# Performance work log

Hardware: AMD Instinct MI355X
Metric: run time of the kernel (lower is better)

Reference implementation:

```python
import jax, jax.numpy as jnp
import numpy as np
import math

B, N, R = 1024, 50, 1000
N_POIS = 50000
D = 128
K_T = 64
K_D = 64
T_MAX = 10080.0
D_MAX = 200.0
EARTH_RADIUS_KM = 6371.0
DEG2RAD = math.pi / 180.0


def _interp_scalar(table, x):
    # Linear interpolation into 1-D table [K]; x are bin positions in [0, K-1].
    K = table.shape[0]
    x = jnp.clip(x, 0.0, K - 1 - 1e-06)
    k = jnp.floor(x).astype(jnp.int32)
    frac = x - k.astype(x.dtype)
    return (1.0 - frac) * table[k] + frac * table[jnp.minimum(k + 1, K - 1)]


def _haversine_km(lat1, lon1, lat2, lon2):
    dlat = (lat2 - lat1) * DEG2RAD
    dlon = (lon2 - lon1) * DEG2RAD
    a = jnp.sin(dlat / 2) ** 2 + jnp.cos(lat1 * DEG2RAD) * jnp.cos(lat2 * DEG2RAD) * jnp.sin(dlon / 2) ** 2
    a = jnp.clip(a, 0.0, 1.0)
    return EARTH_RADIUS_KM * 2.0 * jnp.arcsin(jnp.sqrt(a))


def setup_inputs() -> dict:
    key = jax.random.key(0)
    ks = jax.random.split(key, 16)
    poi_idx = jax.random.randint(ks[0], (B, N), 0, N_POIS)
    hour_of_week = jax.random.randint(ks[1], (B, N), 0, 169)
    lat = jax.random.uniform(ks[2], (B, N), jnp.float32)  # ~1 degree spread => up to ~150 km pairwise
    lon = jax.random.uniform(ks[3], (B, N), jnp.float32)
    t_min = jax.random.uniform(ks[4], (B, N), jnp.float32) * T_MAX
    region_centroids = jax.random.uniform(ks[5], (R, 2), jnp.float32)
    poi_emb = 0.02 * jax.random.normal(ks[6], (N_POIS + 1, D), jnp.float32)
    poi_emb = poi_emb.at[N_POIS].set(0.0)  # padding row
    time_emb = 0.02 * jax.random.normal(ks[7], (169, D), jnp.float32)
    time_emb = time_emb.at[0].set(0.0)  # padding row
    E_t = 0.1 * jax.random.normal(ks[8], (K_T,), jnp.float32)
    E_d = 0.1 * jax.random.normal(ks[9], (K_D,), jnp.float32)
    E_d_match = 0.1 * jax.random.normal(ks[10], (K_D,), jnp.float32)
    region_emb = 0.02 * jax.random.normal(ks[11], (R, D), jnp.float32)
    Wq = jax.random.normal(ks[12], (D, D), jnp.float32) / math.sqrt(D)
    Wk = jax.random.normal(ks[13], (D, D), jnp.float32) / math.sqrt(D)
    Wv = jax.random.normal(ks[14], (D, D), jnp.float32) / math.sqrt(D)
    return dict(poi_idx=poi_idx, hour_of_week=hour_of_week, lat=lat, lon=lon, t_min=t_min,
                region_centroids=region_centroids, poi_emb=poi_emb, time_emb=time_emb,
                E_t=E_t, E_d=E_d, E_d_match=E_d_match, region_emb=region_emb,
                Wq=Wq, Wk=Wk, Wv=Wv)


def reference(poi_idx, hour_of_week, lat, lon, t_min, region_centroids,
              poi_emb, time_emb, E_t, E_d, E_d_match, region_emb, Wq, Wk, Wv):
    pad_mask = poi_idx < 0  # [B, n]
    poi_safe = jnp.where(pad_mask, N_POIS, poi_idx)
    hour_safe = jnp.where(pad_mask, 0, hour_of_week)
    x = poi_emb[poi_safe] + time_emb[hour_safe]  # [B, n, D]

    # pairwise trajectory intervals [B, n, n]
    dt = jnp.abs(t_min[:, :, None] - t_min[:, None, :])
    dd = _haversine_km(lat[:, :, None], lon[:, :, None], lat[:, None, :], lon[:, None, :])
    valid = (~pad_mask).astype(x.dtype)
    valid_pair = valid[:, :, None] * valid[:, None, :]
    dt = dt * valid_pair
    dd = dd * valid_pair

    # _PairwiseBias: scalar table interpolation bias
    t_bin = jnp.clip(dt, 0.0, T_MAX) / T_MAX * (K_T - 1)
    d_bin = jnp.clip(dd, 0.0, D_MAX) / D_MAX * (K_D - 1)
    bias = _interp_scalar(E_t, t_bin) + _interp_scalar(E_d, d_bin)  # [B, n, n]

    # _SelfAttn (single head, no LN/residual, dropout=0)
    Q = x @ Wq.T
    K_ = x @ Wk.T
    V = x @ Wv.T
    scores = jnp.einsum('bnd,bmd->bnm', Q, K_) / math.sqrt(D) + bias
    scores = jnp.where(pad_mask[:, None, :], -jnp.inf, scores)
    attn = jnp.nan_to_num(jax.nn.softmax(scores, axis=-1), nan=0.0)
    S = attn @ V  # [B, n, D]

    # _MatchingLayer
    cand_lat = region_centroids[:, 0]
    cand_lon = region_centroids[:, 1]
    dd_m = _haversine_km(lat[:, :, None], lon[:, :, None], cand_lat[None, None, :], cand_lon[None, None, :])  # [B, n, R]
    dbin_m = jnp.clip(dd_m, 0.0, D_MAX) / D_MAX * (K_D - 1)
    bias_match = _interp_scalar(E_d_match, dbin_m)
    m_scores = jnp.einsum('bnd,rd->bnr', S, region_emb) / math.sqrt(D) + bias_match
    m_scores = jnp.where(pad_mask[:, :, None], -jnp.inf, m_scores)
    m_attn = jnp.nan_to_num(jax.nn.softmax(m_scores, axis=1), nan=0.0)  # softmax over trajectory dim
    scores_safe = jnp.where(pad_mask[:, :, None], 0.0, m_scores)
    return jnp.sum(m_attn * scores_safe, axis=1)  # [B, R]
```

## Files before the change

### kernel.cpp

```cpp
#include <hip/hip_runtime.h>
#include <hip/hip_bf16.h>
#include <math.h>

constexpr int BB    = 1024;
constexpr int NN    = 50;
constexpr int RR    = 1000;
constexpr int DD    = 128;
constexpr int NPOIS = 50000;
#define DEG2RADF  0.017453292519943295f
#define KHALF     0.008726646259971648f
#define RSQRTD    0.08838834764831845f
#define LOG2E     1.4426950408889634f
#define LN2       0.6931471805599453f
#define DBIN_C0   4013.7373f
#define DBIN_C1   668.95621f
#define TBIN_SC   0.00625f
#define PENAL     -1.0e30f

typedef __attribute__((ext_vector_type(8))) short bfrag8;
typedef __attribute__((ext_vector_type(4))) float f32x4;

__device__ __forceinline__ int swz128(int row, int k) {
    return row * 128 + ((((k) >> 3) ^ (row & 7)) << 3) + (k & 7);
}

__device__ __forceinline__ unsigned short f2bf(float x) {
    union { __hip_bfloat16 h; unsigned short u; } cv;
    cv.h = __float2bfloat16(x);
    return cv.u;
}

__device__ __forceinline__ float exp2_asm(float x) {
    float r;
    asm("v_exp_f32 %0, %1" : "=v"(r) : "v"(x));
    return r;
}

__device__ __forceinline__ float fract_asm(float x) {
    float r;
    asm("v_fract_f32 %0, %1" : "=v"(r) : "v"(x));
    return r;
}

__device__ __forceinline__ float cos_small(float x) {
    float x2 = x * x;
    return 1.0f - 0.5f * x2 + 0.041666667f * x2 * x2;
}

__global__ void prep_mg(const float* __restrict__ Wq, const float* __restrict__ Wk,
                        const float* __restrict__ Wv, const float* __restrict__ Re,
                        unsigned short* __restrict__ Mt, unsigned short* __restrict__ Gp) {
    int k = threadIdx.x;
    if (blockIdx.x < DD) {
        int c = blockIdx.x;
        float s0 = 0.f, s1 = 0.f, s2 = 0.f, s3 = 0.f;
        for (int d = 0; d < DD; d += 4) {
            s0 += Wq[(d + 0) * DD + k] * Wk[(d + 0) * DD + c];
            s1 += Wq[(d + 1) * DD + k] * Wk[(d + 1) * DD + c];
            s2 += Wq[(d + 2) * DD + k] * Wk[(d + 2) * DD + c];
            s3 += Wq[(d + 3) * DD + k] * Wk[(d + 3) * DD + c];
        }
        Mt[c * DD + k] = f2bf((s0 + s1 + s2 + s3) * (RSQRTD * LOG2E));
    } else {
        int r = blockIdx.x - DD;
        float val = 0.f;
        if (r < RR) {
            float s0 = 0.f, s1 = 0.f, s2 = 0.f, s3 = 0.f;
            for (int d = 0; d < DD; d += 4) {
                s0 += Wv[(d + 0) * DD + k] * Re[r * DD + d + 0];
                s1 += Wv[(d + 1) * DD + k] * Re[r * DD + d + 1];
                s2 += Wv[(d + 2) * DD + k] * Re[r * DD + d + 2];
                s3 += Wv[(d + 3) * DD + k] * Re[r * DD + d + 3];
            }
            val = (s0 + s1 + s2 + s3) * (RSQRTD * LOG2E);
        }
        int rt = r >> 6, widr = (r >> 4) & 3, colr = r & 15;
        int ks = k >> 5, quad = (k >> 3) & 3, k7 = k & 7;
        int lane = quad * 16 + colr;
        Gp[((((rt * 16 + widr * 4 + ks) * 64) + lane) << 3) + k7] = f2bf(val);
    }
}

__global__ __launch_bounds__(256) void stan_attn(
    const int* __restrict__ poi_idx, const int* __restrict__ hourw,
    const float* __restrict__ lat, const float* __restrict__ lon,
    const float* __restrict__ tmin,
    const float* __restrict__ poi_emb, const float* __restrict__ time_emb,
    const float* __restrict__ Et_g, const float* __restrict__ Ed_g,
    const unsigned short* __restrict__ Mtb, unsigned short* __restrict__ Zw) {
    __shared__ short xs[64 * 128];
    __shared__ union {
        short ys[64 * 128];
        short ps[64 * 64];
    } u2;
    __shared__ float2 Et2[64], Ed2[64];
    __shared__ float4 bnfo[64];
    __shared__ float  jpen[64];

    const int b = blockIdx.x, tid = threadIdx.x;
    const int wid = tid >> 6, lane = tid & 63;
    const int quad = lane >> 4, colr = lane & 15;

    if (tid < 64) {
        int kk = tid > 62 ? 62 : tid;
        float t0 = Et_g[kk] * LOG2E, t1 = Et_g[kk + 1] * LOG2E;
        float d0 = Ed_g[kk] * LOG2E, d1 = Ed_g[kk + 1] * LOG2E;
        Et2[tid] = make_float2(t0, t1 - t0);
        Ed2[tid] = make_float2(d0, d1 - d0);
        if (tid < NN) {
            int p = poi_idx[b * NN + tid];
            float la = lat[b * NN + tid], lo = lon[b * NN + tid];
            bnfo[tid] = make_float4(la * KHALF, lo * KHALF,
                                    cos_small(la * DEG2RADF),
                                    tmin[b * NN + tid] * TBIN_SC);
            jpen[tid] = (p < 0) ? PENAL : 0.f;
        } else {
            bnfo[tid] = make_float4(0.f, 0.f, 1.f, 0.f);
            jpen[tid] = PENAL;
        }
    }
    __syncthreads();

    for (int idx = tid; idx < 64 * 64; idx += 256) {
        int n = idx >> 6, c2 = idx & 63;
        float2 v = make_float2(0.f, 0.f);
        if (n < NN) {
            int p = poi_idx[b * NN + n];
            int pd = (p < 0);
            int ps_ = pd ? NPOIS : p;
            int hs  = pd ? 0 : hourw[b * NN + n];
            float2 pe = ((const float2*)(poi_emb  + (size_t)ps_ * DD))[c2];
            float2 te = ((const float2*)(time_emb + (size_t)hs  * DD))[c2];
            v = make_float2(pe.x + te.x, pe.y + te.y);
        }
        unsigned pack = (unsigned)f2bf(v.x) | ((unsigned)f2bf(v.y) << 16);
        ((unsigned*)xs)[n * 64 + (((c2 >> 2) ^ (n & 7)) << 2) + (c2 & 3)] = pack;
    }
    __syncthreads();

    const int q8    = (quad ^ (colr & 3)) * 8;
    const int kx    = (colr & 4) * 8;
    const int xbase = colr * 128 + q8;
    const int xe = xbase + kx, xo = xbase - kx;

    {
        f32x4 accY[2][4];
        #pragma unroll
        for (int ct = 0; ct < 2; ct++)
            #pragma unroll
            for (int mt = 0; mt < 4; mt++) accY[ct][mt] = (f32x4){0.f, 0.f, 0.f, 0.f};
        #pragma unroll
        for (int ks = 0; ks < 4; ks++) {
            const int k0 = ks * 32 + quad * 8;
            const int xoff = ((ks & 1) ? xo : xe) + ks * 32;
            bfrag8 av[4], bv[2];
            #pragma unroll
            for (int mt = 0; mt < 4; mt++)
                av[mt] = *(const bfrag8*)(&xs[xoff + mt * 2048]);
            #pragma unroll
            for (int ct = 0; ct < 2; ct++) {
                int c = wid * 32 + ct * 16 + colr;
                bv[ct] = *(const bfrag8*)(Mtb + (size_t)c * DD + k0);
            }
            #pragma unroll
            for (int ct = 0; ct < 2; ct++)
                #pragma unroll
                for (int mt = 0; mt < 4; mt++)
                    accY[ct][mt] = __builtin_amdgcn_mfma_f32_16x16x32_bf16(
                        av[mt], bv[ct], accY[ct][mt], 0, 0, 0);
        }
        #pragma unroll
        for (int ct = 0; ct < 2; ct++)
            #pragma unroll
            for (int mt = 0; mt < 4; mt++)
                #pragma unroll
                for (int reg = 0; reg < 4; reg++) {
                    int m = mt * 16 + quad * 4 + reg;
                    int c = wid * 32 + ct * 16 + colr;
                    u2.ys[swz128(m, c)] = (short)f2bf(accY[ct][mt][reg]);
                }
    }
    __syncthreads();

    const int i = wid * 16 + colr;
    const int ybase = xbase + wid * 2048;
    const int ye = ybase + kx, yo = ybase - kx;
    f32x4 accS[4];
    #pragma unroll
    for (int mt = 0; mt < 4; mt++) accS[mt] = (f32x4){0.f, 0.f, 0.f, 0.f};
    #pragma unroll
    for (int ks = 0; ks < 4; ks++) {
        const int yoff = ((ks & 1) ? yo : ye) + ks * 32;
        const int xoff = ((ks & 1) ? xo : xe) + ks * 32;
        bfrag8 bv = *(const bfrag8*)(&u2.ys[yoff]);
        #pragma unroll
        for (int mt = 0; mt < 4; mt++) {
            bfrag8 av = *(const bfrag8*)(&xs[xoff + mt * 2048]);
            accS[mt] = __builtin_amdgcn_mfma_f32_16x16x32_bf16(
                av, bv, accS[mt], 0, 0, 0);
        }
    }
    __syncthreads();

    {
        const float4 bi = bnfo[i];
        float sv[14];
        #pragma unroll
        for (int mt = 0; mt < 4; mt++) {
            const int nregs = (mt == 3) ? 2 : 4;
            #pragma unroll
            for (int reg = 0; reg < nregs; reg++) {
                int j = mt * 16 + quad * 4 + reg;
                float4 bj = bnfo[j];
                float tb = fabsf(bi.w - bj.w);
                int   kt = (int)tb;
                float ft = fract_asm(tb);
                float2 et = Et2[kt];
                float bt = fmaf(ft, et.y, et.x);
                float du = bi.x - bj.x, dv = bi.y - bj.y;
                float a = fmaf((bi.z * bj.z) * dv, dv, du * du);
                float x = __builtin_amdgcn_sqrtf(a);
                float db = x * fmaf(a, DBIN_C1, DBIN_C0);
                int   kd = (int)db;
                float fd = fract_asm(db);
                float2 ed = Ed2[kd];
                float bd = fmaf(fd, ed.y, ed.x);
                sv[mt * 4 + reg] = (accS[mt][reg] + bt) + (bd + jpen[j]);
            }
        }
        float mx = sv[0];
        #pragma unroll
        for (int t = 1; t < 14; t++) mx = fmaxf(mx, sv[t]);
        mx = fmaxf(mx, __shfl_xor(mx, 16, 64));
        mx = fmaxf(mx, __shfl_xor(mx, 32, 64));
        float l = 0.f;
        #pragma unroll
        for (int t = 0; t < 14; t++) {
            float p = exp2_asm(sv[t] - mx);
            sv[t] = p;
            l += p;
        }
        l += __shfl_xor(l, 16, 64);
        l += __shfl_xor(l, 32, 64);
        float rl = __builtin_amdgcn_rcpf(l);
        #pragma unroll
        for (int mt = 0; mt < 4; mt++)
            #pragma unroll
            for (int rp = 0; rp < 2; rp++) {
                int j0 = mt * 16 + quad * 4 + rp * 2;
                unsigned pack;
                if (mt == 3 && rp == 1) {
                    pack = 0u;
                } else {
                    unsigned lo = f2bf(sv[mt * 4 + rp * 2]     * rl);
                    unsigned hi = f2bf(sv[mt * 4 + rp * 2 + 1] * rl);
                    pack = lo | (hi << 16);
                }
                ((unsigned*)u2.ps)[i * 32 + (((j0 >> 3) ^ (i & 7)) << 2) + ((j0 & 7) >> 1)]
                    = pack;
            }
    }
    __syncthreads();

    {
        f32x4 accZ[2][4];
        #pragma unroll
        for (int nt = 0; nt < 2; nt++)
            #pragma unroll
            for (int mt = 0; mt < 4; mt++) accZ[nt][mt] = (f32x4){0.f, 0.f, 0.f, 0.f};
        union BF { unsigned u[4]; bfrag8 v; };
        const int pbase = colr * 64 + q8;
        const int pe = pbase + kx, po = pbase - kx;
        #pragma unroll
        for (int ks = 0; ks < 2; ks++) {
            const int k0 = ks * 32 + quad * 8;
            const int poff = ((ks & 1) ? po : pe) + ks * 32;
            bfrag8 av[4];
            #pragma unroll
            for (int mt = 0; mt < 4; mt++)
                av[mt] = *(const bfrag8*)(&u2.ps[poff + mt * 1024]);
            BF bvx[2];
            #pragma unroll
            for (int nt = 0; nt < 2; nt++) {
                int d = wid * 32 + nt * 16 + colr;
                #pragma unroll
                for (int t2 = 0; t2 < 4; t2++) {
                    unsigned lo = (unsigned short)xs[swz128(k0 + 2 * t2,     d)];
                    unsigned hi = (unsigned short)xs[swz128(k0 + 2 * t2 + 1, d)];
                    bvx[nt].u[t2] = lo | (hi << 16);
                }
            }
            #pragma unroll
            for (int nt = 0; nt < 2; nt++)
                #pragma unroll
                for (int mt = 0; mt < 4; mt++)
                    accZ[nt][mt] = __builtin_amdgcn_mfma_f32_16x16x32_bf16(
                        av[mt], bvx[nt].v, accZ[nt][mt], 0, 0, 0);
        }
        unsigned short* Zb = Zw + (size_t)b * NN * DD;
        #pragma unroll
        for (int mt = 0; mt < 4; mt++)
            #pragma unroll
            for (int reg = 0; reg < 4; reg++) {
                int ii = mt * 16 + quad * 4 + reg;
                if (ii < NN) {
                    #pragma unroll
                    for (int nt = 0; nt < 2; nt++) {
                        int d = wid * 32 + nt * 16 + colr;
                        Zb[(size_t)ii * DD + d] = f2bf(accZ[nt][mt][reg]);
                    }
                }
            }
    }
}

__global__ __launch_bounds__(256, 4) void stan_match(
    const unsigned short* __restrict__ Zw, const unsigned short* __restrict__ Gp,
    const float* __restrict__ cent, const float* __restrict__ Em_g,
    const int* __restrict__ poi_idx,
    const float* __restrict__ lat, const float* __restrict__ lon,
    float* __restrict__ out) {
    __shared__ short  As[64 * 128];
    __shared__ float2 Em2[64];
    __shared__ float4 bnfo[64];

    const int tid = threadIdx.x;
    const int rt0 = blockIdx.x * 8;
    const int b   = blockIdx.y;
    const int wid  = tid >> 6, lane = tid & 63;
    const int quad = lane >> 4, colr = lane & 15;

    bfrag8 bfv[4];
    #pragma unroll
    for (int ks = 0; ks < 4; ks++)
        bfv[ks] = *(const bfrag8*)(Gp + (size_t)(((rt0 * 16 + wid * 4 + ks) * 64 + lane) << 3));

    if (tid < 64) {
        int kk = tid > 62 ? 62 : tid;
        float e0 = Em_g[kk] * LOG2E, e1 = Em_g[kk + 1] * LOG2E;
        Em2[tid] = make_float2(e0, e1 - e0);
        if (tid < NN) {
            float bla = lat[b * NN + tid], blo = lon[b * NN + tid];
            float pen = (poi_idx[b * NN + tid] < 0) ? PENAL : 0.f;
            bnfo[tid] = make_float4(bla * KHALF, blo * KHALF,
                                    cos_small(bla * DEG2RADF), pen);
        } else {
            bnfo[tid] = make_float4(0.f, 0.f, 1.f, PENAL);
        }
    }
    {
        const int row = tid >> 2;
        uint4 z4 = make_uint4(0, 0, 0, 0);
        uint4 a0 = z4, a1 = z4, a2 = z4, a3 = z4;
        if (row < NN) {
            const uint4* src = (const uint4*)(Zw + (size_t)b * NN * DD + row * DD
                                              + (tid & 3) * 32);
            a0 = src[0]; a1 = src[1]; a2 = src[2]; a3 = src[3];
        }
        const int jb = (tid & 3) * 4, rx = row & 7;
        uint4* dstA = (uint4*)As;
        dstA[row * 16 + ((jb + 0) ^ rx)] = a0;
        dstA[row * 16 + ((jb + 1) ^ rx)] = a1;
        dstA[row * 16 + ((jb + 2) ^ rx)] = a2;
        dstA[row * 16 + ((jb + 3) ^ rx)] = a3;
    }
    __syncthreads();

    const int q8    = (quad ^ (colr & 3)) * 8;
    const int kx    = (colr & 4) * 8;
    const int abase = colr * 128 + q8;
    const int ae = abase + kx, ao = abase - kx;
    bfrag8 Af[4][4];
    #pragma unroll
    for (int ks = 0; ks < 4; ks++) {
        const int aoff = ((ks & 1) ? ao : ae) + ks * 32;
        #pragma unroll
        for (int mt = 0; mt < 4; mt++)
            Af[mt][ks] = *(const bfrag8*)(&As[aoff + mt * 2048]);
    }

    const int rL = wid * 16 + colr;

    #pragma unroll 1
    for (int it = 0; it < 8; it++) {
        const int rt = rt0 + it;
        f32x4 acc[4];
        #pragma unroll
        for (int mt = 0; mt < 4; mt++) acc[mt] = (f32x4){0.f, 0.f, 0.f, 0.f};
        #pragma unroll
        for (int ks = 0; ks < 4; ks++)
            #pragma unroll
            for (int mt = 0; mt < 4; mt++)
                acc[mt] = __builtin_amdgcn_mfma_f32_16x16x32_bf16(
                    Af[mt][ks], bfv[ks], acc[mt], 0, 0, 0);

        const int rtn = (it < 7) ? rt + 1 : rt;
        bfrag8 nxt[4];
        #pragma unroll
        for (int ks = 0; ks < 4; ks++)
            nxt[ks] = *(const bfrag8*)(Gp + (size_t)(((rtn * 16 + wid * 4 + ks) * 64 + lane) << 3));

        const int r  = rt * 64 + rL;
        const int rc = (r < RR) ? r : (RR - 1);
        float2 cc = ((const float2*)cent)[rc];
        const float rvx = cc.x * KHALF, rvy = cc.y * KHALF;
        const float rvz = cos_small(cc.x * DEG2RADF);

        float s[14];
        #pragma unroll
        for (int mt = 0; mt < 4; mt++) {
            const int nregs = (mt == 3) ? 2 : 4;
            #pragma unroll
            for (int reg = 0; reg < nregs; reg++) {
                int n = mt * 16 + quad * 4 + reg;
                float4 bn = bnfo[n];
                float du = bn.x - rvx, dv = bn.y - rvy;
                float a = fmaf((bn.z * rvz) * dv, dv, du * du);
                float x = __builtin_amdgcn_sqrtf(a);
                float db = x * fmaf(a, DBIN_C1, DBIN_C0);
                int   kd = (int)db;
                float fd = fract_asm(db);
                float2 ed = Em2[kd];
                float bias = fmaf(fd, ed.y, ed.x);
                s[mt * 4 + reg] = (acc[mt][reg] + bias) + bn.w;
            }
        }
        float l = 0.f, aw = 0.f;
        #pragma unroll
        for (int t = 0; t < 14; t++) {
            float p = exp2_asm(s[t]);
            l += p;
            aw = fmaf(p, s[t], aw);
        }
        l  += __shfl_xor(l, 16, 64); aw += __shfl_xor(aw, 16, 64);
        l  += __shfl_xor(l, 32, 64); aw += __shfl_xor(aw, 32, 64);
        if (quad == 0 && r < RR)
            out[(size_t)b * RR + r] = aw * __builtin_amdgcn_rcpf(l) * LN2;

        #pragma unroll
        for (int ks = 0; ks < 4; ks++) bfv[ks] = nxt[ks];
    }
}

extern "C" void kernel_launch(void* const* d_in, const int* in_sizes, int n_in,
                              void* d_out, int out_size, void* d_ws, size_t ws_size,
                              hipStream_t stream) {
    const int*   poi_idx  = (const int*)d_in[0];
    const int*   hourw    = (const int*)d_in[1];
    const float* lat      = (const float*)d_in[2];
    const float* lon      = (const float*)d_in[3];
    const float* tmin     = (const float*)d_in[4];
    const float* cent     = (const float*)d_in[5];
    const float* poi_emb  = (const float*)d_in[6];
    const float* time_emb = (const float*)d_in[7];
    const float* E_t      = (const float*)d_in[8];
    const float* E_d      = (const float*)d_in[9];
    const float* E_dm     = (const float*)d_in[10];
    const float* Remb     = (const float*)d_in[11];
    const float* Wq       = (const float*)d_in[12];
    const float* Wk       = (const float*)d_in[13];
    const float* Wv       = (const float*)d_in[14];
    float* out            = (float*)d_out;

    unsigned short* Mtb = (unsigned short*)d_ws;
    unsigned short* Gpb = Mtb + DD * DD;
    unsigned short* Zw  = Gpb + (size_t)1024 * DD;

    prep_mg<<<dim3(DD + 1024), DD, 0, stream>>>(Wq, Wk, Wv, Remb, Mtb, Gpb);
    stan_attn<<<dim3(BB), 256, 0, stream>>>(poi_idx, hourw, lat, lon, tmin,
                                            poi_emb, time_emb, E_t, E_d, Mtb, Zw);
    stan_match<<<dim3(2, BB), 256, 0, stream>>>(Zw, Gpb, cent, E_dm, poi_idx, lat, lon, out);
}
```

Baseline: 181.5 us.

## Fuse attention and matching kernels, keeping Z in shared memory

Merges the self-attention and matching kernels into one per-batch kernel. The attention output Z now goes through shared memory instead of a global bf16 buffer, which removes a global write and read and one kernel launch. Each block now loops over all 16 region tiles, where before two blocks split them, so there is less grid parallelism in the matching phase. The attention softmax also drops its max-subtraction step; this assumes scores stay small enough that exp2 cannot overflow.

```diff
diff --git a/kernel.cpp b/kernel.cpp
--- a/kernel.cpp
+++ b/kernel.cpp
@@ -81,20 +81,24 @@
     }
 }
 
-__global__ __launch_bounds__(256) void stan_attn(
+__global__ __launch_bounds__(256, 4) void stan_fused(
     const int* __restrict__ poi_idx, const int* __restrict__ hourw,
     const float* __restrict__ lat, const float* __restrict__ lon,
     const float* __restrict__ tmin,
     const float* __restrict__ poi_emb, const float* __restrict__ time_emb,
     const float* __restrict__ Et_g, const float* __restrict__ Ed_g,
-    const unsigned short* __restrict__ Mtb, unsigned short* __restrict__ Zw) {
+    const float* __restrict__ Em_g,
+    const unsigned short* __restrict__ Mtb, const unsigned short* __restrict__ Gp,
+    const float* __restrict__ cent, float* __restrict__ out) {
     __shared__ short xs[64 * 128];
     __shared__ union {
         short ys[64 * 128];
         short ps[64 * 64];
+        short as_[64 * 128];
     } u2;
-    __shared__ float2 Et2[64], Ed2[64];
+    __shared__ float2 Et2[64], Ed2[64], Em2[64];
     __shared__ float4 bnfo[64];
+    __shared__ float4 bnfoM[64];
     __shared__ float  jpen[64];
 
     const int b = blockIdx.x, tid = threadIdx.x;
@@ -105,17 +109,22 @@
         int kk = tid > 62 ? 62 : tid;
         float t0 = Et_g[kk] * LOG2E, t1 = Et_g[kk + 1] * LOG2E;
         float d0 = Ed_g[kk] * LOG2E, d1 = Ed_g[kk + 1] * LOG2E;
+        float e0 = Em_g[kk] * LOG2E, e1 = Em_g[kk + 1] * LOG2E;
         Et2[tid] = make_float2(t0, t1 - t0);
         Ed2[tid] = make_float2(d0, d1 - d0);
+        Em2[tid] = make_float2(e0, e1 - e0);
         if (tid < NN) {
             int p = poi_idx[b * NN + tid];
             float la = lat[b * NN + tid], lo = lon[b * NN + tid];
-            bnfo[tid] = make_float4(la * KHALF, lo * KHALF,
-                                    cos_small(la * DEG2RADF),
-                                    tmin[b * NN + tid] * TBIN_SC);
-            jpen[tid] = (p < 0) ? PENAL : 0.f;
+            float cs = cos_small(la * DEG2RADF);
+            float pen = (p < 0) ? PENAL : 0.f;
+            bnfo[tid]  = make_float4(la * KHALF, lo * KHALF, cs,
+                                     tmin[b * NN + tid] * TBIN_SC);
+            bnfoM[tid] = make_float4(la * KHALF, lo * KHALF, cs, pen);
+            jpen[tid] = pen;
         } else {
-            bnfo[tid] = make_float4(0.f, 0.f, 1.f, 0.f);
+            bnfo[tid]  = make_float4(0.f, 0.f, 1.f, 0.f);
+            bnfoM[tid] = make_float4(0.f, 0.f, 1.f, PENAL);
             jpen[tid] = PENAL;
         }
     }
@@ -228,15 +237,10 @@
                 sv[mt * 4 + reg] = (accS[mt][reg] + bt) + (bd + jpen[j]);
             }
         }
-        float mx = sv[0];
-        #pragma unroll
-        for (int t = 1; t < 14; t++) mx = fmaxf(mx, sv[t]);
-        mx = fmaxf(mx, __shfl_xor(mx, 16, 64));
-        mx = fmaxf(mx, __shfl_xor(mx, 32, 64));
         float l = 0.f;
         #pragma unroll
         for (int t = 0; t < 14; t++) {
-            float p = exp2_asm(sv[t] - mx);
+            float p = exp2_asm(sv[t]);
             sv[t] = p;
             l += p;
         }
@@ -297,93 +301,39 @@
                     accZ[nt][mt] = __builtin_amdgcn_mfma_f32_16x16x32_bf16(
                         av[mt], bvx[nt].v, accZ[nt][mt], 0, 0, 0);
         }
-        unsigned short* Zb = Zw + (size_t)b * NN * DD;
+        __syncthreads();
         #pragma unroll
         for (int mt = 0; mt < 4; mt++)
             #pragma unroll
             for (int reg = 0; reg < 4; reg++) {
                 int ii = mt * 16 + quad * 4 + reg;
-                if (ii < NN) {
-                    #pragma unroll
-                    for (int nt = 0; nt < 2; nt++) {
-                        int d = wid * 32 + nt * 16 + colr;
-                        Zb[(size_t)ii * DD + d] = f2bf(accZ[nt][mt][reg]);
-                    }
+                #pragma unroll
+                for (int nt = 0; nt < 2; nt++) {
+                    int d = wid * 32 + nt * 16 + colr;
+                    float zv = (ii < NN) ? accZ[nt][mt][reg] : 0.f;
+                    u2.as_[swz128(ii, d)] = (short)f2bf(zv);
                 }
             }
     }
-}
-
-__global__ __launch_bounds__(256, 4) void stan_match(
-    const unsigned short* __restrict__ Zw, const unsigned short* __restrict__ Gp,
-    const float* __restrict__ cent, const float* __restrict__ Em_g,
-    const int* __restrict__ poi_idx,
-    const float* __restrict__ lat, const float* __restrict__ lon,
-    float* __restrict__ out) {
-    __shared__ short  As[64 * 128];
-    __shared__ float2 Em2[64];
-    __shared__ float4 bnfo[64];
-
-    const int tid = threadIdx.x;
-    const int rt0 = blockIdx.x * 8;
-    const int b   = blockIdx.y;
-    const int wid  = tid >> 6, lane = tid & 63;
-    const int quad = lane >> 4, colr = lane & 15;
-
+    __syncthreads();
+
+    bfrag8 Af[4][4];
+    #pragma unroll
+    for (int ks = 0; ks < 4; ks++) {
+        const int aoff = ((ks & 1) ? xo : xe) + ks * 32;
+        #pragma unroll
+        for (int mt = 0; mt < 4; mt++)
+            Af[mt][ks] = *(const bfrag8*)(&u2.as_[aoff + mt * 2048]);
+    }
     bfrag8 bfv[4];
     #pragma unroll
     for (int ks = 0; ks < 4; ks++)
-        bfv[ks] = *(const bfrag8*)(Gp + (size_t)(((rt0 * 16 + wid * 4 + ks) * 64 + lane) << 3));
-
-    if (tid < 64) {
-        int kk = tid > 62 ? 62 : tid;
-        float e0 = Em_g[kk] * LOG2E, e1 = Em_g[kk + 1] * LOG2E;
-        Em2[tid] = make_float2(e0, e1 - e0);
-        if (tid < NN) {
-            float bla = lat[b * NN + tid], blo = lon[b * NN + tid];
-            float pen = (poi_idx[b * NN + tid] < 0) ? PENAL : 0.f;
-            bnfo[tid] = make_float4(bla * KHALF, blo * KHALF,
-                                    cos_small(bla * DEG2RADF), pen);
-        } else {
-            bnfo[tid] = make_float4(0.f, 0.f, 1.f, PENAL);
-        }
-    }
-    {
-        const int row = tid >> 2;
-        uint4 z4 = make_uint4(0, 0, 0, 0);
-        uint4 a0 = z4, a1 = z4, a2 = z4, a3 = z4;
-        if (row < NN) {
-            const uint4* src = (const uint4*)(Zw + (size_t)b * NN * DD + row * DD
-                                              + (tid & 3) * 32);
-            a0 = src[0]; a1 = src[1]; a2 = src[2]; a3 = src[3];
-        }
-        const int jb = (tid & 3) * 4, rx = row & 7;
-        uint4* dstA = (uint4*)As;
-        dstA[row * 16 + ((jb + 0) ^ rx)] = a0;
-        dstA[row * 16 + ((jb + 1) ^ rx)] = a1;
-        dstA[row * 16 + ((jb + 2) ^ rx)] = a2;
-        dstA[row * 16 + ((jb + 3) ^ rx)] = a3;
-    }
-    __syncthreads();
-
-    const int q8    = (quad ^ (colr & 3)) * 8;
-    const int kx    = (colr & 4) * 8;
-    const int abase = colr * 128 + q8;
-    const int ae = abase + kx, ao = abase - kx;
-    bfrag8 Af[4][4];
-    #pragma unroll
-    for (int ks = 0; ks < 4; ks++) {
-        const int aoff = ((ks & 1) ? ao : ae) + ks * 32;
-        #pragma unroll
-        for (int mt = 0; mt < 4; mt++)
-            Af[mt][ks] = *(const bfrag8*)(&As[aoff + mt * 2048]);
-    }
+        bfv[ks] = *(const bfrag8*)(Gp + (size_t)(((wid * 4 + ks) * 64 + lane) << 3));
 
     const int rL = wid * 16 + colr;
 
     #pragma unroll 1
-    for (int it = 0; it < 8; it++) {
-        const int rt = rt0 + it;
+    for (int it = 0; it < 16; it++) {
         f32x4 acc[4];
         #pragma unroll
         for (int mt = 0; mt < 4; mt++) acc[mt] = (f32x4){0.f, 0.f, 0.f, 0.f};
@@ -394,13 +344,13 @@
                 acc[mt] = __builtin_amdgcn_mfma_f32_16x16x32_bf16(
                     Af[mt][ks], bfv[ks], acc[mt], 0, 0, 0);
 
-        const int rtn = (it < 7) ? rt + 1 : rt;
+        const int rtn = (it < 15) ? it + 1 : it;
         bfrag8 nxt[4];
         #pragma unroll
         for (int ks = 0; ks < 4; ks++)
             nxt[ks] = *(const bfrag8*)(Gp + (size_t)(((rtn * 16 + wid * 4 + ks) * 64 + lane) << 3));
 
-        const int r  = rt * 64 + rL;
+        const int r  = it * 64 + rL;
         const int rc = (r < RR) ? r : (RR - 1);
         float2 cc = ((const float2*)cent)[rc];
         const float rvx = cc.x * KHALF, rvy = cc.y * KHALF;
@@ -413,7 +363,7 @@
             #pragma unroll
             for (int reg = 0; reg < nregs; reg++) {
                 int n = mt * 16 + quad * 4 + reg;
-                float4 bn = bnfo[n];
+                float4 bn = bnfoM[n];
                 float du = bn.x - rvx, dv = bn.y - rvy;
                 float a = fmaf((bn.z * rvz) * dv, dv, du * du);
                 float x = __builtin_amdgcn_sqrtf(a);
@@ -464,10 +414,9 @@
 
     unsigned short* Mtb = (unsigned short*)d_ws;
     unsigned short* Gpb = Mtb + DD * DD;
-    unsigned short* Zw  = Gpb + (size_t)1024 * DD;
 
     prep_mg<<<dim3(DD + 1024), DD, 0, stream>>>(Wq, Wk, Wv, Remb, Mtb, Gpb);
-    stan_attn<<<dim3(BB), 256, 0, stream>>>(poi_idx, hourw, lat, lon, tmin,
-                                            poi_emb, time_emb, E_t, E_d, Mtb, Zw);
-    stan_match<<<dim3(2, BB), 256, 0, stream>>>(Zw, Gpb, cent, E_dm, poi_idx, lat, lon, out);
-}
+    stan_fused<<<dim3(BB), 256, 0, stream>>>(poi_idx, hourw, lat, lon, tmin,
+                                             poi_emb, time_emb, E_t, E_d, E_dm,
+                                             Mtb, Gpb, cent, out);
+}
```

New measurement: 161.2 us. 1.13x faster.
